# Kernel tuning notes

Measured on AMD Instinct MI355X. Metric: run time of the kernel, lower is better.

Reference implementation:

```python
import jax, jax.numpy as jnp
import numpy as np


def setup_inputs() -> dict:
    key = jax.random.key(0)
    k1, k2 = jax.random.split(key)
    N, D = 8192, 200
    preds = jax.random.normal(k1, (N, 1, 1, D), dtype=jnp.float32)
    labels = jax.random.randint(k2, (N,), 0, 64, dtype=jnp.int64)
    return {"preds": preds, "labels": labels}


def reference(preds, labels):
    # preds: (N,1,1,200) -> flatten to (N,200); torch.dist is the L2 norm of the
    # elementwise difference over the whole tensor.
    N = preds.shape[0]
    x = preds.reshape(N, -1).astype(jnp.float32)
    sq = jnp.sum(x * x, axis=-1)                      # (N,)
    gram = x @ x.T                                    # (N,N)
    d2 = sq[:, None] + sq[None, :] - 2.0 * gram       # squared pairwise dist
    eye = jnp.eye(N, dtype=bool)
    # keep diagonal out of the sqrt (it is skipped by the i==j continue)
    d2_safe = jnp.where(eye, 1.0, jnp.maximum(d2, 0.0))
    dist = jnp.sqrt(d2_safe)                          # (N,N)
    sign = jnp.where(labels[:, None] == labels[None, :], 1.0, -1.0)
    sign = jnp.where(eye, 0.0, sign)
    # each pred_loss[i] is a (1,1,200) tensor filled with the scalar s_i,
    # so the final mean over the stack equals mean_i(s_i).
    per_i = jnp.sum(sign * dist, axis=1)              # (N,)
    return jnp.mean(per_i)
```

## Files before the change

### kernel.cpp

```cpp
#include <hip/hip_runtime.h>
#include <hip/hip_bf16.h>
#include <hip/hip_fp8.h>

#define N 8192
#define D 200
#define KP 232
#define NSTEP 7
#define NB 64
#define NBLK 512
#define NPART (NBLK * 4)
#define PANEL (128 * KP)

typedef float f32x4 __attribute__((ext_vector_type(4)));
#define AS3 __attribute__((address_space(3)))
#define AS1 __attribute__((address_space(1)))

__global__ __launch_bounds__(256) void prep_kernel(
    const float* __restrict__ x, const int* __restrict__ labels,
    unsigned char* __restrict__ xb, float* __restrict__ sq,
    int* __restrict__ lab) {
  int row = blockIdx.x * 4 + (threadIdx.x >> 6);
  int lane = threadIdx.x & 63;
  const float* xr = x + (size_t)row * D;
  unsigned char* xbr = xb + (size_t)row * KP;
  int k0 = lane * 4;
  float4 f = {0.f, 0.f, 0.f, 0.f};
  if (k0 < D) f = *(const float4*)(xr + k0);
  float s = 0.f;
  unsigned char q[4];
  float ff[4] = {f.x, f.y, f.z, f.w};
#pragma unroll
  for (int c = 0; c < 4; ++c) {
    float v = (k0 + c < D) ? ff[c] : 0.f;
    __hip_fp8_e4m3 h(v);
    q[c] = h.__x;
    float fb = (float)h;
    s += fb * fb;
  }
  if (k0 < KP) *(uchar4*)(xbr + k0) = *(uchar4*)q;
#pragma unroll
  for (int m = 32; m; m >>= 1) s += __shfl_xor(s, m);
  if (lane == 0) {
    sq[row] = s;
    lab[row] = labels[row];
  }
}

__global__ __launch_bounds__(256) void gram_kernel(
    const unsigned char* __restrict__ xb, const float* __restrict__ sq,
    const int* __restrict__ lab, double* __restrict__ partial) {
  __shared__ __align__(16) unsigned char sA[PANEL];
  __shared__ __align__(16) unsigned char sB[PANEL];

  const int t = threadIdx.x;
  const int b = blockIdx.x;
  const int q = b >> 4, s = b & 15;
  const int row2 = 63 - q;
  const int n1 = 64 - q;

  const int wid = t >> 6, lane = t & 63;
  const int col = lane & 15, quad = lane >> 4;
  const int waveM = (wid >> 1) * 64, waveN = (wid & 1) * 64;

  auto stage = [&](const unsigned char* g, unsigned char* sh) {
#pragma unroll
    for (int c = 0; c < 7; ++c) {
      int off = c * 4096 + t * 16;
      __builtin_amdgcn_global_load_lds((const AS1 void*)(g + off),
                                       (AS3 void*)(sh + off), 16, 0, 0);
    }
    if (t < 64) {
      int off = 28672 + t * 16;
      __builtin_amdgcn_global_load_lds((const AS1 void*)(g + off),
                                       (AS3 void*)(sh + off), 16, 0, 0);
    }
  };

  int idx = s;
  int bi = (idx < n1) ? q : row2;
  int bj = (idx < n1) ? q + idx : row2 + (idx - n1);
  stage(xb + (size_t)bi * PANEL, sA);
  stage(xb + (size_t)bj * PANEL, sB);
  __syncthreads();

  float tot = 0.f;
  while (true) {
    f32x4 acc[4][4] = {};
#pragma unroll
    for (int step = 0; step < NSTEP; ++step) {
      long a[4], bf[4];
#pragma unroll
      for (int mi = 0; mi < 4; ++mi)
        a[mi] = *(const long*)(sA + (waveM + mi * 16 + col) * KP + step * 32 + quad * 8);
#pragma unroll
      for (int ni = 0; ni < 4; ++ni)
        bf[ni] = *(const long*)(sB + (waveN + ni * 16 + col) * KP + step * 32 + quad * 8);
#pragma unroll
      for (int mi = 0; mi < 4; ++mi)
#pragma unroll
        for (int ni = 0; ni < 4; ++ni)
          acc[mi][ni] = __builtin_amdgcn_mfma_f32_16x16x32_fp8_fp8(
              a[mi], bf[ni], acc[mi][ni], 0, 0, 0);
    }
    __syncthreads();

    const int nidx = idx + 16;
    const bool more = (nidx < 65);
    int nbi = 0, nbj = 0;
    if (more) {
      nbi = (nidx < n1) ? q : row2;
      nbj = (nidx < n1) ? q + nidx : row2 + (nidx - n1);
      if (nbi != bi) stage(xb + (size_t)nbi * PANEL, sA);
      stage(xb + (size_t)nbj * PANEL, sB);
    }

    const int i0 = bi * 128 + waveM, j0 = bj * 128 + waveN;
    int labj[4];
    float sqj[4];
#pragma unroll
    for (int ni = 0; ni < 4; ++ni) {
      int j = j0 + ni * 16 + col;
      labj[ni] = lab[j];
      sqj[ni] = sq[j];
    }
    float rs = 0.f;
    if (bi != bj) {
#pragma unroll
      for (int mi = 0; mi < 4; ++mi) {
#pragma unroll
        for (int r = 0; r < 4; ++r) {
          int i = i0 + mi * 16 + quad * 4 + r;
          float sqi = sq[i];
          int li = lab[i];
#pragma unroll
          for (int ni = 0; ni < 4; ++ni) {
            float g = acc[mi][ni][r];
            float d2 = fmaxf(fmaf(-2.f, g, sqi + sqj[ni]), 0.f);
            float dist = __builtin_amdgcn_sqrtf(d2);
            rs += (li == labj[ni]) ? dist : -dist;
          }
        }
      }
      tot += 2.f * rs;
    } else {
#pragma unroll
      for (int mi = 0; mi < 4; ++mi) {
#pragma unroll
        for (int r = 0; r < 4; ++r) {
          int i = i0 + mi * 16 + quad * 4 + r;
          float sqi = sq[i];
          int li = lab[i];
#pragma unroll
          for (int ni = 0; ni < 4; ++ni) {
            int j = j0 + ni * 16 + col;
            float g = acc[mi][ni][r];
            float d2 = fmaxf(fmaf(-2.f, g, sqi + sqj[ni]), 0.f);
            float dist = __builtin_amdgcn_sqrtf(d2);
            float c = (li == labj[ni]) ? dist : -dist;
            rs += (i == j) ? 0.f : c;
          }
        }
      }
      tot += rs;
    }

    if (!more) break;
    bi = nbi; bj = nbj; idx = nidx;
    __syncthreads();
  }

#pragma unroll
  for (int m = 32; m; m >>= 1) tot += __shfl_xor(tot, m);
  if (lane == 0) partial[b * 4 + wid] = (double)tot;
}

__global__ __launch_bounds__(256) void reduce_kernel(
    const double* __restrict__ partial, float* __restrict__ out) {
  __shared__ double wsum[4];
  double s = 0.0;
  for (int i = threadIdx.x; i < NPART; i += 256) s += partial[i];
#pragma unroll
  for (int m = 32; m; m >>= 1) s += __shfl_xor(s, m);
  if ((threadIdx.x & 63) == 0) wsum[threadIdx.x >> 6] = s;
  __syncthreads();
  if (threadIdx.x == 0)
    out[0] = (float)((wsum[0] + wsum[1] + wsum[2] + wsum[3]) / (double)N);
}

extern "C" void kernel_launch(void* const* d_in, const int* in_sizes, int n_in,
                              void* d_out, int out_size, void* d_ws, size_t ws_size,
                              hipStream_t stream) {
  const float* x = (const float*)d_in[0];
  const int* labels = (const int*)d_in[1];
  char* ws = (char*)d_ws;
  unsigned char* xb = (unsigned char*)ws;
  float* sq = (float*)(ws + (size_t)N * KP);
  int* lab = (int*)(ws + (size_t)N * KP + (size_t)N * 4);
  double* partial = (double*)(ws + (size_t)N * KP + (size_t)N * 8);
  float* out = (float*)d_out;

  prep_kernel<<<N / 4, 256, 0, stream>>>(x, labels, xb, sq, lab);
  gram_kernel<<<NBLK, 256, 0, stream>>>(xb, sq, lab, partial);
  reduce_kernel<<<1, 256, 0, stream>>>(partial, out);
}
```

Measured before the change: 83.45 us.

## Use one-tile-per-block 64x64 gram tiles and fuse final reduction via atomics

Replaces the persistent 512-block loop over 128x128 tiles with 8256 blocks, each computing one 64x64 upper-triangle tile, with a launch bound asking for more resident blocks. The final reduce kernel is removed: each block atomically adds its partial sum into one of 256 double cells, and the last block (found with an atomic counter) sums the cells and writes the output. Prep zeroes the cells and counter. This is meant to improve load balance and latency hiding and to drop a launch, at the cost of staging more data per FLOP from smaller tiles and adding atomic traffic.

After: 225.0 us. +169.7%, slower.

```diff
diff --git a/kernel.cpp b/kernel.cpp
--- a/kernel.cpp
+++ b/kernel.cpp
@@ -1,15 +1,16 @@
 #include <hip/hip_runtime.h>
-#include <hip/hip_bf16.h>
 #include <hip/hip_fp8.h>
 
 #define N 8192
 #define D 200
 #define KP 232
 #define NSTEP 7
-#define NB 64
-#define NBLK 512
-#define NPART (NBLK * 4)
-#define PANEL (128 * KP)
+#define TB 64
+#define NT 128
+#define TPP 129
+#define NBLK (64 * TPP)
+#define PANEL (TB * KP)
+#define NCELL 256
 
 typedef float f32x4 __attribute__((ext_vector_type(4)));
 #define AS3 __attribute__((address_space(3)))
@@ -18,7 +19,12 @@
 __global__ __launch_bounds__(256) void prep_kernel(
     const float* __restrict__ x, const int* __restrict__ labels,
     unsigned char* __restrict__ xb, float* __restrict__ sq,
-    int* __restrict__ lab) {
+    int* __restrict__ lab, double* __restrict__ cells,
+    unsigned int* __restrict__ counter) {
+  if (blockIdx.x == 0) {
+    cells[threadIdx.x] = 0.0;
+    if (threadIdx.x == 0) *counter = 0u;
+  }
   int row = blockIdx.x * 4 + (threadIdx.x >> 6);
   int lane = threadIdx.x & 63;
   const float* xr = x + (size_t)row * D;
@@ -46,145 +52,130 @@
   }
 }
 
-__global__ __launch_bounds__(256) void gram_kernel(
+__global__ __launch_bounds__(256, 5) void gram_kernel(
     const unsigned char* __restrict__ xb, const float* __restrict__ sq,
-    const int* __restrict__ lab, double* __restrict__ partial) {
+    const int* __restrict__ lab, double* __restrict__ cells,
+    unsigned int* __restrict__ counter, float* __restrict__ out) {
   __shared__ __align__(16) unsigned char sA[PANEL];
   __shared__ __align__(16) unsigned char sB[PANEL];
+  __shared__ double wsum[4];
+  __shared__ int lastFlag;
 
   const int t = threadIdx.x;
   const int b = blockIdx.x;
-  const int q = b >> 4, s = b & 15;
-  const int row2 = 63 - q;
-  const int n1 = 64 - q;
-
-  const int wid = t >> 6, lane = t & 63;
-  const int col = lane & 15, quad = lane >> 4;
-  const int waveM = (wid >> 1) * 64, waveN = (wid & 1) * 64;
+  const int q = b / TPP, idx = b % TPP;
+  const int n1 = NT - q;
+  const int I = (idx < n1) ? q : NT - 1 - q;
+  const int J = (idx < n1) ? q + idx : (NT - 1 - q) + (idx - n1);
 
   auto stage = [&](const unsigned char* g, unsigned char* sh) {
 #pragma unroll
-    for (int c = 0; c < 7; ++c) {
+    for (int c = 0; c < 3; ++c) {
       int off = c * 4096 + t * 16;
       __builtin_amdgcn_global_load_lds((const AS1 void*)(g + off),
                                        (AS3 void*)(sh + off), 16, 0, 0);
     }
-    if (t < 64) {
-      int off = 28672 + t * 16;
+    if (t < 160) {
+      int off = 12288 + t * 16;
       __builtin_amdgcn_global_load_lds((const AS1 void*)(g + off),
                                        (AS3 void*)(sh + off), 16, 0, 0);
     }
   };
-
-  int idx = s;
-  int bi = (idx < n1) ? q : row2;
-  int bj = (idx < n1) ? q + idx : row2 + (idx - n1);
-  stage(xb + (size_t)bi * PANEL, sA);
-  stage(xb + (size_t)bj * PANEL, sB);
+  stage(xb + (size_t)I * PANEL, sA);
+  stage(xb + (size_t)J * PANEL, sB);
   __syncthreads();
 
-  float tot = 0.f;
-  while (true) {
-    f32x4 acc[4][4] = {};
+  const int wid = t >> 6, lane = t & 63;
+  const int col = lane & 15, quad = lane >> 4;
+  const int waveM = (wid >> 1) * 32, waveN = (wid & 1) * 32;
+
+  f32x4 acc[2][2] = {};
 #pragma unroll
-    for (int step = 0; step < NSTEP; ++step) {
-      long a[4], bf[4];
+  for (int step = 0; step < NSTEP; ++step) {
+    long a[2], bf[2];
 #pragma unroll
-      for (int mi = 0; mi < 4; ++mi)
-        a[mi] = *(const long*)(sA + (waveM + mi * 16 + col) * KP + step * 32 + quad * 8);
+    for (int mi = 0; mi < 2; ++mi)
+      a[mi] = *(const long*)(sA + (waveM + mi * 16 + col) * KP + step * 32 + quad * 8);
 #pragma unroll
-      for (int ni = 0; ni < 4; ++ni)
-        bf[ni] = *(const long*)(sB + (waveN + ni * 16 + col) * KP + step * 32 + quad * 8);
+    for (int ni = 0; ni < 2; ++ni)
+      bf[ni] = *(const long*)(sB + (waveN + ni * 16 + col) * KP + step * 32 + quad * 8);
 #pragma unroll
-      for (int mi = 0; mi < 4; ++mi)
+    for (int mi = 0; mi < 2; ++mi)
 #pragma unroll
-        for (int ni = 0; ni < 4; ++ni)
-          acc[mi][ni] = __builtin_amdgcn_mfma_f32_16x16x32_fp8_fp8(
-              a[mi], bf[ni], acc[mi][ni], 0, 0, 0);
-    }
-    __syncthreads();
+      for (int ni = 0; ni < 2; ++ni)
+        acc[mi][ni] = __builtin_amdgcn_mfma_f32_16x16x32_fp8_fp8(
+            a[mi], bf[ni], acc[mi][ni], 0, 0, 0);
+  }
 
-    const int nidx = idx + 16;
-    const bool more = (nidx < 65);
-    int nbi = 0, nbj = 0;
-    if (more) {
-      nbi = (nidx < n1) ? q : row2;
-      nbj = (nidx < n1) ? q + nidx : row2 + (nidx - n1);
-      if (nbi != bi) stage(xb + (size_t)nbi * PANEL, sA);
-      stage(xb + (size_t)nbj * PANEL, sB);
-    }
-
-    const int i0 = bi * 128 + waveM, j0 = bj * 128 + waveN;
-    int labj[4];
-    float sqj[4];
+  const int i0 = I * TB + waveM, j0 = J * TB + waveN;
+  int labj[2];
+  float sqj[2];
 #pragma unroll
-    for (int ni = 0; ni < 4; ++ni) {
-      int j = j0 + ni * 16 + col;
-      labj[ni] = lab[j];
-      sqj[ni] = sq[j];
-    }
-    float rs = 0.f;
-    if (bi != bj) {
+  for (int ni = 0; ni < 2; ++ni) {
+    int j = j0 + ni * 16 + col;
+    labj[ni] = lab[j];
+    sqj[ni] = sq[j];
+  }
+  float rs = 0.f, tot;
+  if (I != J) {
 #pragma unroll
-      for (int mi = 0; mi < 4; ++mi) {
+    for (int mi = 0; mi < 2; ++mi)
 #pragma unroll
-        for (int r = 0; r < 4; ++r) {
-          int i = i0 + mi * 16 + quad * 4 + r;
-          float sqi = sq[i];
-          int li = lab[i];
+      for (int r = 0; r < 4; ++r) {
+        int i = i0 + mi * 16 + quad * 4 + r;
+        float sqi = sq[i];
+        int li = lab[i];
 #pragma unroll
-          for (int ni = 0; ni < 4; ++ni) {
-            float g = acc[mi][ni][r];
-            float d2 = fmaxf(fmaf(-2.f, g, sqi + sqj[ni]), 0.f);
-            float dist = __builtin_amdgcn_sqrtf(d2);
-            rs += (li == labj[ni]) ? dist : -dist;
-          }
+        for (int ni = 0; ni < 2; ++ni) {
+          float g = acc[mi][ni][r];
+          float d2 = fmaxf(fmaf(-2.f, g, sqi + sqj[ni]), 0.f);
+          float dist = __builtin_amdgcn_sqrtf(d2);
+          rs += (li == labj[ni]) ? dist : -dist;
         }
       }
-      tot += 2.f * rs;
-    } else {
+    tot = 2.f * rs;
+  } else {
 #pragma unroll
-      for (int mi = 0; mi < 4; ++mi) {
+    for (int mi = 0; mi < 2; ++mi)
 #pragma unroll
-        for (int r = 0; r < 4; ++r) {
-          int i = i0 + mi * 16 + quad * 4 + r;
-          float sqi = sq[i];
-          int li = lab[i];
+      for (int r = 0; r < 4; ++r) {
+        int i = i0 + mi * 16 + quad * 4 + r;
+        float sqi = sq[i];
+        int li = lab[i];
 #pragma unroll
-          for (int ni = 0; ni < 4; ++ni) {
-            int j = j0 + ni * 16 + col;
-            float g = acc[mi][ni][r];
-            float d2 = fmaxf(fmaf(-2.f, g, sqi + sqj[ni]), 0.f);
-            float dist = __builtin_amdgcn_sqrtf(d2);
-            float c = (li == labj[ni]) ? dist : -dist;
-            rs += (i == j) ? 0.f : c;
-          }
+        for (int ni = 0; ni < 2; ++ni) {
+          int j = j0 + ni * 16 + col;
+          float g = acc[mi][ni][r];
+          float d2 = fmaxf(fmaf(-2.f, g, sqi + sqj[ni]), 0.f);
+          float dist = __builtin_amdgcn_sqrtf(d2);
+          float c = (li == labj[ni]) ? dist : -dist;
+          rs += (i == j) ? 0.f : c;
         }
       }
-      tot += rs;
-    }
-
-    if (!more) break;
-    bi = nbi; bj = nbj; idx = nidx;
-    __syncthreads();
+    tot = rs;
   }
 
 #pragma unroll
   for (int m = 32; m; m >>= 1) tot += __shfl_xor(tot, m);
-  if (lane == 0) partial[b * 4 + wid] = (double)tot;
-}
-
-__global__ __launch_bounds__(256) void reduce_kernel(
-    const double* __restrict__ partial, float* __restrict__ out) {
-  __shared__ double wsum[4];
-  double s = 0.0;
-  for (int i = threadIdx.x; i < NPART; i += 256) s += partial[i];
+  if (lane == 0) wsum[wid] = (double)tot;
+  __syncthreads();
+  if (t == 0) {
+    double bs = wsum[0] + wsum[1] + wsum[2] + wsum[3];
+    atomicAdd(&cells[b & (NCELL - 1)], bs);
+    __threadfence();
+    unsigned int old = atomicAdd(counter, 1u);
+    lastFlag = (old == NBLK - 1) ? 1 : 0;
+  }
+  __syncthreads();
+  if (lastFlag) {
+    double sacc = atomicAdd(&cells[t], 0.0);
 #pragma unroll
-  for (int m = 32; m; m >>= 1) s += __shfl_xor(s, m);
-  if ((threadIdx.x & 63) == 0) wsum[threadIdx.x >> 6] = s;
-  __syncthreads();
-  if (threadIdx.x == 0)
-    out[0] = (float)((wsum[0] + wsum[1] + wsum[2] + wsum[3]) / (double)N);
+    for (int m = 32; m; m >>= 1) sacc += __shfl_xor(sacc, m);
+    if (lane == 0) wsum[wid] = sacc;
+    __syncthreads();
+    if (t == 0)
+      out[0] = (float)((wsum[0] + wsum[1] + wsum[2] + wsum[3]) / (double)N);
+  }
 }
 
 extern "C" void kernel_launch(void* const* d_in, const int* in_sizes, int n_in,
@@ -196,10 +187,11 @@
   unsigned char* xb = (unsigned char*)ws;
   float* sq = (float*)(ws + (size_t)N * KP);
   int* lab = (int*)(ws + (size_t)N * KP + (size_t)N * 4);
-  double* partial = (double*)(ws + (size_t)N * KP + (size_t)N * 8);
+  double* cells = (double*)(ws + (size_t)N * KP + (size_t)N * 8);
+  unsigned int* counter =
+      (unsigned int*)(ws + (size_t)N * KP + (size_t)N * 8 + NCELL * 8);
   float* out = (float*)d_out;
 
-  prep_kernel<<<N / 4, 256, 0, stream>>>(x, labels, xb, sq, lab);
-  gram_kernel<<<NBLK, 256, 0, stream>>>(xb, sq, lab, partial);
-  reduce_kernel<<<1, 256, 0, stream>>>(partial, out);
+  prep_kernel<<<N / 4, 256, 0, stream>>>(x, labels, xb, sq, lab, cells, counter);
+  gram_kernel<<<NBLK, 256, 0, stream>>>(xb, sq, lab, cells, counter, out);
 }
```

## Give each wave an independent 64x64 tile loading fp8 operands from global

Applied to the files above, without the earlier changes.

Replaces the block-level 128x128 tiles staged through LDS with a per-wave 64x64 tile decomposition over the upper triangle (128x129/2 tiles). Each wave reads its A and B fragments directly from global memory or cache, with no LDS staging and no barriers, and there is no loop over tiles per block. This removes synchronisation and LDS overhead and spreads work across many more blocks. In exchange, each wave issues uncoalesced 8-byte global loads and loses operand reuse across the waves of a block.

Result: slower. 104.2 us (+24.8%).

```diff
diff --git a/kernel.cpp b/kernel.cpp
--- a/kernel.cpp
+++ b/kernel.cpp
@@ -1,19 +1,19 @@
 #include <hip/hip_runtime.h>
-#include <hip/hip_bf16.h>
 #include <hip/hip_fp8.h>
 
 #define N 8192
 #define D 200
 #define KP 232
 #define NSTEP 7
-#define NB 64
-#define NBLK 512
-#define NPART (NBLK * 4)
-#define PANEL (128 * KP)
+#define TB 64
+#define NT 128
+#define TPP 129
+#define NTILE (64 * TPP)
+#define NBLK (NTILE / 4)
+#define PANEL (TB * KP)
+#define NPART NTILE
 
 typedef float f32x4 __attribute__((ext_vector_type(4)));
-#define AS3 __attribute__((address_space(3)))
-#define AS1 __attribute__((address_space(1)))
 
 __global__ __launch_bounds__(256) void prep_kernel(
     const float* __restrict__ x, const int* __restrict__ labels,
@@ -49,129 +49,87 @@
 __global__ __launch_bounds__(256) void gram_kernel(
     const unsigned char* __restrict__ xb, const float* __restrict__ sq,
     const int* __restrict__ lab, double* __restrict__ partial) {
-  __shared__ __align__(16) unsigned char sA[PANEL];
-  __shared__ __align__(16) unsigned char sB[PANEL];
+  const int t = threadIdx.x;
+  const int wid = t >> 6, lane = t & 63;
+  const int w = blockIdx.x * 4 + wid;
+  const int q = w / TPP, idx = w - q * TPP;
+  const int n1 = NT - q;
+  const int I = (idx < n1) ? q : NT - 1 - q;
+  const int J = (idx < n1) ? q + idx : (NT - 1 - q) + (idx - n1);
+  const int col = lane & 15, quad = lane >> 4;
 
-  const int t = threadIdx.x;
-  const int b = blockIdx.x;
-  const int q = b >> 4, s = b & 15;
-  const int row2 = 63 - q;
-  const int n1 = 64 - q;
+  const unsigned char* Ab = xb + (size_t)I * PANEL + col * KP + quad * 8;
+  const unsigned char* Bb = xb + (size_t)J * PANEL + col * KP + quad * 8;
 
-  const int wid = t >> 6, lane = t & 63;
-  const int col = lane & 15, quad = lane >> 4;
-  const int waveM = (wid >> 1) * 64, waveN = (wid & 1) * 64;
-
-  auto stage = [&](const unsigned char* g, unsigned char* sh) {
+  f32x4 acc[4][4] = {};
 #pragma unroll
-    for (int c = 0; c < 7; ++c) {
-      int off = c * 4096 + t * 16;
-      __builtin_amdgcn_global_load_lds((const AS1 void*)(g + off),
-                                       (AS3 void*)(sh + off), 16, 0, 0);
-    }
-    if (t < 64) {
-      int off = 28672 + t * 16;
-      __builtin_amdgcn_global_load_lds((const AS1 void*)(g + off),
-                                       (AS3 void*)(sh + off), 16, 0, 0);
-    }
-  };
-
-  int idx = s;
-  int bi = (idx < n1) ? q : row2;
-  int bj = (idx < n1) ? q + idx : row2 + (idx - n1);
-  stage(xb + (size_t)bi * PANEL, sA);
-  stage(xb + (size_t)bj * PANEL, sB);
-  __syncthreads();
-
-  float tot = 0.f;
-  while (true) {
-    f32x4 acc[4][4] = {};
+  for (int step = 0; step < NSTEP; ++step) {
+    long a[4], bf[4];
 #pragma unroll
-    for (int step = 0; step < NSTEP; ++step) {
-      long a[4], bf[4];
+    for (int mi = 0; mi < 4; ++mi)
+      a[mi] = *(const long*)(Ab + mi * (16 * KP) + step * 32);
 #pragma unroll
-      for (int mi = 0; mi < 4; ++mi)
-        a[mi] = *(const long*)(sA + (waveM + mi * 16 + col) * KP + step * 32 + quad * 8);
+    for (int ni = 0; ni < 4; ++ni)
+      bf[ni] = *(const long*)(Bb + ni * (16 * KP) + step * 32);
+#pragma unroll
+    for (int mi = 0; mi < 4; ++mi)
 #pragma unroll
       for (int ni = 0; ni < 4; ++ni)
-        bf[ni] = *(const long*)(sB + (waveN + ni * 16 + col) * KP + step * 32 + quad * 8);
+        acc[mi][ni] = __builtin_amdgcn_mfma_f32_16x16x32_fp8_fp8(
+            a[mi], bf[ni], acc[mi][ni], 0, 0, 0);
+  }
+
+  const int i0 = I * TB, j0 = J * TB;
+  int labj[4];
+  float sqj[4];
 #pragma unroll
-      for (int mi = 0; mi < 4; ++mi)
+  for (int ni = 0; ni < 4; ++ni) {
+    int j = j0 + ni * 16 + col;
+    labj[ni] = lab[j];
+    sqj[ni] = sq[j];
+  }
+  float rs = 0.f, tot;
+  if (I != J) {
 #pragma unroll
-        for (int ni = 0; ni < 4; ++ni)
-          acc[mi][ni] = __builtin_amdgcn_mfma_f32_16x16x32_fp8_fp8(
-              a[mi], bf[ni], acc[mi][ni], 0, 0, 0);
-    }
-    __syncthreads();
-
-    const int nidx = idx + 16;
-    const bool more = (nidx < 65);
-    int nbi = 0, nbj = 0;
-    if (more) {
-      nbi = (nidx < n1) ? q : row2;
-      nbj = (nidx < n1) ? q + nidx : row2 + (nidx - n1);
-      if (nbi != bi) stage(xb + (size_t)nbi * PANEL, sA);
-      stage(xb + (size_t)nbj * PANEL, sB);
-    }
-
-    const int i0 = bi * 128 + waveM, j0 = bj * 128 + waveN;
-    int labj[4];
-    float sqj[4];
+    for (int mi = 0; mi < 4; ++mi)
 #pragma unroll
-    for (int ni = 0; ni < 4; ++ni) {
-      int j = j0 + ni * 16 + col;
-      labj[ni] = lab[j];
-      sqj[ni] = sq[j];
-    }
-    float rs = 0.f;
-    if (bi != bj) {
+      for (int r = 0; r < 4; ++r) {
+        int i = i0 + mi * 16 + quad * 4 + r;
+        float sqi = sq[i];
+        int li = lab[i];
 #pragma unroll
-      for (int mi = 0; mi < 4; ++mi) {
-#pragma unroll
-        for (int r = 0; r < 4; ++r) {
-          int i = i0 + mi * 16 + quad * 4 + r;
-          float sqi = sq[i];
-          int li = lab[i];
-#pragma unroll
-          for (int ni = 0; ni < 4; ++ni) {
-            float g = acc[mi][ni][r];
-            float d2 = fmaxf(fmaf(-2.f, g, sqi + sqj[ni]), 0.f);
-            float dist = __builtin_amdgcn_sqrtf(d2);
-            rs += (li == labj[ni]) ? dist : -dist;
-          }
+        for (int ni = 0; ni < 4; ++ni) {
+          float g = acc[mi][ni][r];
+          float d2 = fmaxf(fmaf(-2.f, g, sqi + sqj[ni]), 0.f);
+          float dist = __builtin_amdgcn_sqrtf(d2);
+          rs += (li == labj[ni]) ? dist : -dist;
         }
       }
-      tot += 2.f * rs;
-    } else {
+    tot = 2.f * rs;
+  } else {
 #pragma unroll
-      for (int mi = 0; mi < 4; ++mi) {
+    for (int mi = 0; mi < 4; ++mi)
 #pragma unroll
-        for (int r = 0; r < 4; ++r) {
-          int i = i0 + mi * 16 + quad * 4 + r;
-          float sqi = sq[i];
-          int li = lab[i];
+      for (int r = 0; r < 4; ++r) {
+        int i = i0 + mi * 16 + quad * 4 + r;
+        float sqi = sq[i];
+        int li = lab[i];
 #pragma unroll
-          for (int ni = 0; ni < 4; ++ni) {
-            int j = j0 + ni * 16 + col;
-            float g = acc[mi][ni][r];
-            float d2 = fmaxf(fmaf(-2.f, g, sqi + sqj[ni]), 0.f);
-            float dist = __builtin_amdgcn_sqrtf(d2);
-            float c = (li == labj[ni]) ? dist : -dist;
-            rs += (i == j) ? 0.f : c;
-          }
+        for (int ni = 0; ni < 4; ++ni) {
+          int j = j0 + ni * 16 + col;
+          float g = acc[mi][ni][r];
+          float d2 = fmaxf(fmaf(-2.f, g, sqi + sqj[ni]), 0.f);
+          float dist = __builtin_amdgcn_sqrtf(d2);
+          float c = (li == labj[ni]) ? dist : -dist;
+          rs += (i == j) ? 0.f : c;
         }
       }
-      tot += rs;
-    }
-
-    if (!more) break;
-    bi = nbi; bj = nbj; idx = nidx;
-    __syncthreads();
+    tot = rs;
   }
 
 #pragma unroll
   for (int m = 32; m; m >>= 1) tot += __shfl_xor(tot, m);
-  if (lane == 0) partial[b * 4 + wid] = (double)tot;
+  if (lane == 0) partial[w] = (double)tot;
 }
 
 __global__ __launch_bounds__(256) void reduce_kernel(
```
